# Performance work log

Hardware: AMD Instinct MI355X
Metric: run time of the kernel (lower is better)

## Reference

```python
import jax, jax.numpy as jnp
import numpy as np

H = 32          # num attention heads
KVH = 8         # num key/value heads
D = 128         # head dim
THETA = 10000.0


def _rope_tables(kv_len):
    inv_freq = 1.0 / (THETA ** (jnp.arange(0, D, 2, dtype=jnp.float32) / D))  # [D/2]
    t = jnp.arange(kv_len, dtype=jnp.float32)
    freqs = jnp.outer(t, inv_freq)                  # [kv_len, D/2]
    emb = jnp.concatenate([freqs, freqs], axis=-1)  # [kv_len, D]
    return jnp.cos(emb), jnp.sin(emb)


def _rotate_half(x):
    x1, x2 = jnp.split(x, 2, axis=-1)
    return jnp.concatenate([-x2, x1], axis=-1)


def setup_inputs() -> dict:
    key = jax.random.key(0)
    ks = jax.random.split(key, 7)
    B, QL, KVL, HID = 4, 128, 4096, 4096
    hidden_states = jax.random.normal(ks[0], (B, QL, HID), jnp.float32)
    key_states = jax.random.normal(ks[1], (B, KVH, KVL, D), jnp.float32)
    value_states = jax.random.normal(ks[2], (B, KVH, KVL, D), jnp.float32)
    Wq = jax.random.normal(ks[3], (HID, H * D), jnp.float32) * (HID ** -0.5)
    Wo = jax.random.normal(ks[4], (H * D, HID), jnp.float32) * ((H * D) ** -0.5)
    position_ids = jnp.sort(jax.random.randint(ks[5], (B, KVL), 0, KVL), axis=-1).astype(jnp.int64)
    attention_mask = jax.random.randint(ks[6], (B, 1, QL, KVL), 0, 2) == 1
    return {"hidden_states": hidden_states, "key_states": key_states,
            "value_states": value_states, "Wq": Wq, "Wo": Wo,
            "position_ids": position_ids, "attention_mask": attention_mask}


def reference(hidden_states, key_states, value_states, Wq, Wo, position_ids, attention_mask):
    B, QL, HID = hidden_states.shape
    KVL = position_ids.shape[-1]

    # q projection -> [B, H, QL, D]
    q = (hidden_states @ Wq).reshape(B, QL, H, D).transpose(0, 2, 1, 3)

    # RoPE: apply rotation for the single max position per batch to all q positions
    cos, sin = _rope_tables(KVL)                               # [KVL, D]
    pos = jnp.take_along_axis(position_ids,
                              jnp.argmax(position_ids.astype(jnp.int32), axis=1)[:, None],
                              axis=1)                          # [B, 1]
    cos_b = cos[pos][:, None]                                  # [B, 1, 1, D]
    sin_b = sin[pos][:, None]
    q = q * cos_b + _rotate_half(q) * sin_b

    # GQA repeat kv heads -> [B, H, KVL, D]
    groups = H // KVH
    k = jnp.repeat(key_states, groups, axis=1)
    v = jnp.repeat(value_states, groups, axis=1)

    scores = jnp.einsum('bhqd,bhkd->bhqk', q, k) / jnp.sqrt(jnp.float32(D))
    scores = jnp.where(attention_mask, jnp.float32(-10000.0), scores)
    attn = jax.nn.softmax(scores.astype(jnp.float32), axis=-1).astype(q.dtype)

    out = jnp.einsum('bhqk,bhkd->bhqd', attn, v)               # [B, H, QL, D]
    out = out.transpose(0, 2, 1, 3).reshape(B, QL, H * D)
    return out @ Wo
```

## Files before the change

### kernel.cpp

```cpp
#include <hip/hip_runtime.h>
#include <math.h>

typedef __attribute__((ext_vector_type(8))) short bf16x8;
typedef __attribute__((ext_vector_type(4))) float f32x4;
typedef __attribute__((ext_vector_type(4))) short s16x4;
typedef __attribute__((ext_vector_type(4))) int i32x4;

__device__ inline unsigned short f2bf(float x){
  unsigned u = __builtin_bit_cast(unsigned, x);
  u = (u + 0x7FFFu + ((u >> 16) & 1u)) >> 16;
  return (unsigned short)u;
}
__device__ inline unsigned pk2bf(float lo, float hi){
  return (unsigned)f2bf(lo) | ((unsigned)f2bf(hi) << 16);
}

__device__ inline void gl16(const void* g, void* l){
  __builtin_amdgcn_global_load_lds(
      (const __attribute__((address_space(1))) unsigned int*)g,
      (__attribute__((address_space(3))) unsigned int*)l, 16, 0, 0);
}

#define KVLEN 4096
#define QLEN  128
#define NH    32
#define NKVH  8
#define HD    128
#define HIDD  4096
#define NSPLIT 4
#define KVCHUNK (KVLEN / NSPLIT)

__global__ void prep_kernel(const int* __restrict__ pos32,
                            const unsigned int* __restrict__ mask32,
                            float* __restrict__ costab,
                            float* __restrict__ sintab,
                            int* __restrict__ flags){
  int tid = threadIdx.x;
  if (tid < 64){
    unsigned long long bal = __ballot((mask32[tid] & 0xFFFFFF00u) != 0);
    if (tid == 0) flags[0] = (bal != 0) ? 1 : 0;
  }
  int b = tid >> 6, j = tid & 63;
  bool pos64 = (pos32[2*4095 + 1] == 0);
  long long mpos;
  if (pos64) mpos = ((const long long*)pos32)[(size_t)b*KVLEN + KVLEN - 1];
  else       mpos = (long long)pos32[(size_t)b*KVLEN + KVLEN - 1];
  double inv = pow(10000.0, -((double)j) / 64.0);
  double ang = (double)mpos * inv;
  costab[b*64 + j] = (float)cos(ang);
  sintab[b*64 + j] = (float)sin(ang);
}

__global__ __launch_bounds__(256) void maskpack_kernel(const void* __restrict__ mask,
                                                       const int* __restrict__ flags,
                                                       unsigned long long* __restrict__ bits){
  int idx = blockIdx.x * 256 + threadIdx.x;
  bool m8 = (flags[0] != 0);
  bool v = m8 ? (((const unsigned char*)mask)[idx] != 0)
              : (((const int*)mask)[idx] != 0);
  unsigned long long bal = __ballot(v);
  if ((threadIdx.x & 63) == 0) bits[idx >> 6] = bal;
}

__global__ __launch_bounds__(256) void kvprep_kernel(const float* __restrict__ Kg,
                                                     const float* __restrict__ Vg,
                                                     unsigned short* __restrict__ Kswz,
                                                     unsigned short* __restrict__ V2){
  __shared__ alignas(16) char tl[16384];
  int bid = blockIdx.x;
  int tid = threadIdx.x;
  const float* kin = Kg + (size_t)bid * 8192;
  const float* vin = Vg + (size_t)bid * 8192;
  unsigned short* kout = Kswz + (size_t)bid * 8192;
  unsigned short* vout = V2   + (size_t)bid * 8192;
#pragma unroll
  for (int i = 0; i < 4; ++i){
    int c = tid + 256*i;
    int r = c >> 4, d0 = (c & 15) * 8;
    f32x4 x0 = *(const f32x4*)(kin + r*128 + d0);
    f32x4 x1 = *(const f32x4*)(kin + r*128 + d0 + 4);
    bf16x8 s;
#pragma unroll
    for (int t = 0; t < 4; ++t){ s[t] = (short)f2bf(x0[t]); s[t+4] = (short)f2bf(x1[t]); }
    unsigned o = ((unsigned)(r*256 + d0*2)) ^ (((unsigned)r & 7u) << 4);
    *(bf16x8*)(tl + o) = s;
  }
  __syncthreads();
#pragma unroll
  for (int i = 0; i < 4; ++i)
    *(bf16x8*)((char*)kout + tid*16 + i*4096) = *(const bf16x8*)(tl + tid*16 + i*4096);
#pragma unroll
  for (int i = 0; i < 4; ++i){
    int c = tid + 256*i;
    int l16 = c & 15, lk4 = (c >> 4) & 3, ks2 = (c >> 6) & 1, nf8 = c >> 7;
    int d = nf8*16 + l16;
    int kvb = ks2*32 + lk4*8;
    bf16x8 s;
#pragma unroll
    for (int e = 0; e < 8; ++e) s[e] = (short)f2bf(vin[(size_t)(kvb + e)*128 + d]);
    *(bf16x8*)(vout + (size_t)c*8) = s;
  }
}

__global__ __launch_bounds__(256) void wprep_kernel(const float* __restrict__ Wq,
                                                    const float* __restrict__ Wo,
                                                    const float* __restrict__ hidden,
                                                    unsigned short* __restrict__ WqImg,
                                                    unsigned short* __restrict__ WoImg,
                                                    unsigned short* __restrict__ A1img){
  __shared__ alignas(16) char tl[16384];
  int bid = blockIdx.x, tid = threadIdx.x;
  if (bid < 4096){
    const float* W = (bid < 2048) ? Wq : Wo;
    unsigned short* img = (bid < 2048) ? WqImg : WoImg;
    int t = bid & 2047;
    int bn = t >> 6, kt = t & 63;
    char* outB = (char*)img + (size_t)t * 16384;
#pragma unroll
    for (int i = 0; i < 4; ++i){
      int c = tid + 256*i;
      int n = c & 127, kc = c >> 7;
      const float* src = W + (size_t)(kt*64 + kc*8) * HIDD + bn*128 + n;
      bf16x8 s;
#pragma unroll
      for (int e = 0; e < 8; ++e) s[e] = (short)f2bf(src[(size_t)e * HIDD]);
      unsigned off = ((unsigned)(n*128 + kc*16)) ^ (((unsigned)n & 7u) << 4);
      *(bf16x8*)(tl + off) = s;
    }
    __syncthreads();
#pragma unroll
    for (int i = 0; i < 4; ++i)
      *(bf16x8*)(outB + tid*16 + i*4096) = *(const bf16x8*)(tl + tid*16 + i*4096);
  } else {
    int t = bid - 4096;
    int bm = t >> 6, kt = t & 63;
    char* outA = (char*)A1img + (size_t)t * 8192;
#pragma unroll
    for (int i = 0; i < 2; ++i){
      int c = tid + 256*i;
      int m = c >> 3, kc = c & 7;
      const float* src = hidden + (size_t)(bm*64 + m) * HIDD + kt*64 + kc*8;
      f32x4 x0 = *(const f32x4*)src;
      f32x4 x1 = *(const f32x4*)(src + 4);
      bf16x8 s;
#pragma unroll
      for (int e = 0; e < 4; ++e){ s[e] = (short)f2bf(x0[e]); s[e+4] = (short)f2bf(x1[e]); }
      unsigned off = ((unsigned)(m*128 + kc*16)) ^ (((unsigned)m & 7u) << 4);
      *(bf16x8*)(tl + off) = s;
    }
    __syncthreads();
#pragma unroll
    for (int i = 0; i < 2; ++i)
      *(bf16x8*)(outA + tid*16 + i*4096) = *(const bf16x8*)(tl + tid*16 + i*4096);
  }
}

template<int EPI>
__global__ __launch_bounds__(256) void gemm_kernel(const unsigned short* __restrict__ Aimg,
                                                   const unsigned short* __restrict__ Bimg,
                                                   void* __restrict__ C_,
                                                   const float* __restrict__ costab,
                                                   const float* __restrict__ sintab){
  __shared__ alignas(16) char smem[98304];
  int bid = blockIdx.x;
  int bn = (bid & 7) | ((bid >> 6) << 3);
  int bm = (bid >> 3) & 7;
  int tid = threadIdx.x, lane = tid & 63, w = tid >> 6;
  int wm = w >> 1, wn = w & 1;
  int l16 = lane & 15, lk4 = lane >> 4;
  const char* At = (const char*)Aimg + (size_t)bm * 64 * 8192;
  const char* Bt = (const char*)Bimg + (size_t)bn * 64 * 16384;
  f32x4 acc[2][4] = {};

#define GSTAGE(KT, BUF) do { \
    const char* ga_ = At + (size_t)(KT)*8192  + w*2048 + lane*16; \
    const char* gb_ = Bt + (size_t)(KT)*16384 + w*4096 + lane*16; \
    char* la_ = smem + (BUF)*24576 + w*2048; \
    char* lb_ = smem + (BUF)*24576 + 8192 + w*4096; \
    gl16(ga_, la_); gl16(ga_ + 1024, la_ + 1024); \
    _Pragma("unroll") for (int i_ = 0; i_ < 4; ++i_) gl16(gb_ + i_*1024, lb_ + i_*1024); \
  } while(0)

  GSTAGE(0, 0); GSTAGE(1, 1); GSTAGE(2, 2);

  for (int kt = 0; kt < 64; ++kt){
    if (kt + 2 < 64)      asm volatile("s_waitcnt vmcnt(12)" ::: "memory");
    else if (kt + 1 < 64) asm volatile("s_waitcnt vmcnt(6)" ::: "memory");
    else                  asm volatile("s_waitcnt vmcnt(0)" ::: "memory");
    __syncthreads();
    if (kt + 3 < 64) GSTAGE(kt + 3, (kt + 3) & 3);
    const char* Ab = smem + (kt & 3)*24576;
    const char* Bb = Ab + 8192;
    bf16x8 af[2][2];
#pragma unroll
    for (int i = 0; i < 2; ++i)
#pragma unroll
      for (int ks = 0; ks < 2; ++ks){
        unsigned m = (unsigned)(wm*32 + i*16 + l16);
        unsigned off = (m*128u + (unsigned)(ks*64 + lk4*16)) ^ ((m & 7u) << 4);
        af[i][ks] = *(const bf16x8*)(Ab + off);
      }
#pragma unroll
    for (int j = 0; j < 4; ++j)
#pragma unroll
      for (int ks = 0; ks < 2; ++ks){
        unsigned n = (unsigned)(wn*64 + j*16 + l16);
        unsigned off = (n*128u + (unsigned)(ks*64 + lk4*16)) ^ ((n & 7u) << 4);
        bf16x8 bfr = *(const bf16x8*)(Bb + off);
#pragma unroll
        for (int i = 0; i < 2; ++i)
          acc[i][j] = __builtin_amdgcn_mfma_f32_16x16x32_bf16(af[i][ks], bfr, acc[i][j], 0, 0, 0);
      }
  }
#undef GSTAGE

  if (EPI == 0){
    float* C = (float*)C_;
#pragma unroll
    for (int i = 0; i < 2; ++i)
#pragma unroll
      for (int j = 0; j < 4; ++j)
#pragma unroll
        for (int r = 0; r < 4; ++r){
          int row = bm*64 + wm*32 + i*16 + lk4*4 + r;
          int col = bn*128 + wn*64 + j*16 + l16;
          C[(size_t)row * HIDD + col] = acc[i][j][r];
        }
  } else {
    float* etile = (float*)smem;
    __syncthreads();
#pragma unroll
    for (int i = 0; i < 2; ++i)
#pragma unroll
      for (int j = 0; j < 4; ++j)
#pragma unroll
        for (int r = 0; r < 4; ++r){
          int m = wm*32 + i*16 + lk4*4 + r;
          int n = wn*64 + j*16 + l16;
          etile[m*132 + n] = acc[i][j][r];
        }
    __syncthreads();
    unsigned short* Q = (unsigned short*)C_;
    int b = bm >> 1;
    int m2 = tid & 63;
    int dh = tid >> 6;
    int ql = (bm & 1)*64 + m2;
    size_t ob = ((size_t)(b*NH + bn) * QLEN + ql) * HD;
    const float scale = 0.08838834764831845f;
#pragma unroll
    for (int dd = 0; dd < 16; ++dd){
      int d = dh*16 + dd;
      float x1 = etile[m2*132 + d];
      float x2 = etile[m2*132 + d + 64];
      float c = costab[b*64 + d];
      float s = sintab[b*64 + d];
      Q[ob + d]      = f2bf((x1*c - x2*s)*scale);
      Q[ob + d + 64] = f2bf((x2*c + x1*s)*scale);
    }
  }
}

__global__ __launch_bounds__(256, 2) void attn_kernel(const unsigned short* __restrict__ Q,
                                                      const unsigned short* __restrict__ Kswz,
                                                      const unsigned short* __restrict__ V2,
                                                      const unsigned long long* __restrict__ bits,
                                                      float* __restrict__ Opart,
                                                      float* __restrict__ Mpart,
                                                      float* __restrict__ Lpart){
  __shared__ alignas(16) unsigned short Kbuf[2][8192];
  __shared__ alignas(16) unsigned short Vbuf[2][8192];
  int bid = blockIdx.x;
  int g = (bid & 7) | ((bid >> 5) << 3);
  int j = (bid >> 3) & 3;
  int s   = g & 3;
  int kvh = (g >> 2) & 7;
  int b   = g >> 5;
  int h   = kvh * 4 + j;

  int tid = threadIdx.x, lane = tid & 63, w = tid >> 6;
  int l16 = lane & 15, lk4 = lane >> 4;
  int lk4x4 = lk4 * 4;

  bf16x8 qf[2][4];
#pragma unroll
  for (int qg = 0; qg < 2; ++qg){
    const unsigned short* qp = Q + (((size_t)(b*NH + h) * QLEN) + w*32 + qg*16 + l16) * HD;
#pragma unroll
    for (int ks = 0; ks < 4; ++ks)
      qf[qg][ks] = *(const bf16x8*)(qp + ks*32 + lk4*8);
  }
  f32x4 acc_o[2][8] = {};
  float mrun[2] = {-1e30f, -1e30f}, lrun[2] = {0.f, 0.f};

  size_t kvhbase = (size_t)(b*NKVH + kvh) * (KVLEN/64);
  const unsigned short* Ktiles = Kswz + kvhbase * 8192;
  const unsigned short* Vtiles = V2   + kvhbase * 8192;
  size_t qrow0 = (size_t)(b*QLEN + w*32 + l16);

  const int t0 = s * (KVCHUNK/64), t1 = t0 + KVCHUNK/64;
  int srcb0 = (l16 + ((lk4 & 1) << 5)) << 2;
  int srcb1 = srcb0 + 64;

#define STAGE(T, BUF) do { \
    const char* gk_ = (const char*)(Ktiles + (size_t)(T)*8192) + w*4096 + lane*16; \
    const char* gv_ = (const char*)(Vtiles + (size_t)(T)*8192) + w*4096 + lane*16; \
    char* lk_ = (char*)(&Kbuf[BUF][0]) + w*4096; \
    char* lv_ = (char*)(&Vbuf[BUF][0]) + w*4096; \
    _Pragma("unroll") for (int i_ = 0; i_ < 4; ++i_) gl16(gk_ + i_*1024, lk_ + i_*1024); \
    _Pragma("unroll") for (int i_ = 0; i_ < 4; ++i_) gl16(gv_ + i_*1024, lv_ + i_*1024); \
  } while(0)

  STAGE(t0, 0);
  int cur = 0;
  for (int t = t0; t < t1; ++t){
    asm volatile("s_waitcnt vmcnt(0)" ::: "memory");
    __syncthreads();
    if (t + 1 < t1) STAGE(t + 1, cur ^ 1);

    unsigned long long wrd[2];
    wrd[0] = bits[qrow0*64 + (size_t)t];
    wrd[1] = bits[(qrow0 + 16)*64 + (size_t)t];

    f32x4 sacc[2][4] = {};
#pragma unroll
    for (int nf = 0; nf < 4; ++nf){
      int krow = nf*16 + l16;
#pragma unroll
      for (int ks = 0; ks < 4; ++ks){
        unsigned byteoff = ((unsigned)krow*256u + (unsigned)(ks*32 + lk4*8)*2u) ^ (((unsigned)krow & 7u) << 4);
        bf16x8 kf = *(const bf16x8*)((const char*)&Kbuf[cur][0] + byteoff);
        sacc[0][nf] = __builtin_amdgcn_mfma_f32_16x16x32_bf16(kf, qf[0][ks], sacc[0][nf], 0, 0, 0);
        sacc[1][nf] = __builtin_amdgcn_mfma_f32_16x16x32_bf16(kf, qf[1][ks], sacc[1][nf], 0, 0, 0);
      }
    }

    unsigned P32[2][8];
#pragma unroll
    for (int qg = 0; qg < 2; ++qg){
      float p[4][4];
      float pm = -1e30f;
#pragma unroll
      for (int nf = 0; nf < 4; ++nf)
#pragma unroll
        for (int r = 0; r < 4; ++r){
          bool mk = (wrd[qg] >> (nf*16 + lk4x4 + r)) & 1ull;
          float sv = mk ? -10000.f : sacc[qg][nf][r];
          p[nf][r] = sv;
          pm = fmaxf(pm, sv);
        }
      pm = fmaxf(pm, __shfl_xor(pm, 16, 64));
      pm = fmaxf(pm, __shfl_xor(pm, 32, 64));
      float mnew = fmaxf(mrun[qg], pm);
      float corr = __expf(mrun[qg] - mnew);
      mrun[qg] = mnew;
      float ps = 0.f;
#pragma unroll
      for (int nf = 0; nf < 4; ++nf)
#pragma unroll
        for (int r = 0; r < 4; ++r){
          float e = __expf(p[nf][r] - mnew);
          p[nf][r] = e;
          ps += e;
        }
      ps += __shfl_xor(ps, 16, 64);
      ps += __shfl_xor(ps, 32, 64);
      lrun[qg] = lrun[qg]*corr + ps;
#pragma unroll
      for (int nf8 = 0; nf8 < 8; ++nf8)
#pragma unroll
        for (int r = 0; r < 4; ++r) acc_o[qg][nf8][r] *= corr;
#pragma unroll
      for (int nf = 0; nf < 4; ++nf){
        P32[qg][nf*2]     = pk2bf(p[nf][0], p[nf][1]);
        P32[qg][nf*2 + 1] = pk2bf(p[nf][2], p[nf][3]);
      }
    }

    bf16x8 pf[2][2];
    bool hi = lk4 >= 2;
#pragma unroll
    for (int qg = 0; qg < 2; ++qg)
#pragma unroll
      for (int ks2 = 0; ks2 < 2; ++ks2){
        int a0 = __builtin_amdgcn_ds_bpermute(srcb0, (int)P32[qg][ks2*4 + 0]);
        int b0 = __builtin_amdgcn_ds_bpermute(srcb0, (int)P32[qg][ks2*4 + 2]);
        int a1 = __builtin_amdgcn_ds_bpermute(srcb0, (int)P32[qg][ks2*4 + 1]);
        int b1 = __builtin_amdgcn_ds_bpermute(srcb0, (int)P32[qg][ks2*4 + 3]);
        int a2 = __builtin_amdgcn_ds_bpermute(srcb1, (int)P32[qg][ks2*4 + 0]);
        int b2 = __builtin_amdgcn_ds_bpermute(srcb1, (int)P32[qg][ks2*4 + 2]);
        int a3 = __builtin_amdgcn_ds_bpermute(srcb1, (int)P32[qg][ks2*4 + 1]);
        int b3 = __builtin_amdgcn_ds_bpermute(srcb1, (int)P32[qg][ks2*4 + 3]);
        i32x4 wv = { hi ? b0 : a0, hi ? b1 : a1, hi ? b2 : a2, hi ? b3 : a3 };
        pf[qg][ks2] = __builtin_bit_cast(bf16x8, wv);
      }

#pragma unroll
    for (int nf8 = 0; nf8 < 8; ++nf8)
#pragma unroll
      for (int ks2 = 0; ks2 < 2; ++ks2){
        unsigned byteoff = (unsigned)(nf8*2 + ks2)*1024u + (unsigned)lane*16u;
        bf16x8 vf = *(const bf16x8*)((const char*)&Vbuf[cur][0] + byteoff);
        acc_o[0][nf8] = __builtin_amdgcn_mfma_f32_16x16x32_bf16(vf, pf[0][ks2], acc_o[0][nf8], 0, 0, 0);
        acc_o[1][nf8] = __builtin_amdgcn_mfma_f32_16x16x32_bf16(vf, pf[1][ks2], acc_o[1][nf8], 0, 0, 0);
      }
    cur ^= 1;
  }
#undef STAGE

  size_t rowbase = ((size_t)(s*4 + b) * NH + h) * QLEN + w*32 + l16;
#pragma unroll
  for (int qg = 0; qg < 2; ++qg){
    size_t row = rowbase + qg*16;
#pragma unroll
    for (int nf8 = 0; nf8 < 8; ++nf8)
      *(f32x4*)&Opart[row * HD + nf8*16 + lk4x4] = acc_o[qg][nf8];
    if (lk4 == 0){
      Mpart[row] = mrun[qg];
      Lpart[row] = lrun[qg];
    }
  }
}

__global__ __launch_bounds__(256) void combine_kernel(const float* __restrict__ Opart,
                                                      const float* __restrict__ Mpart,
                                                      const float* __restrict__ Lpart,
                                                      unsigned short* __restrict__ A2img){
  int idx = blockIdx.x * 256 + threadIdx.x;
  int d4 = idx & 31;
  int row = idx >> 5;
  const int RS = 4 * NH * QLEN;
  float m[NSPLIT];
#pragma unroll
  for (int s = 0; s < NSPLIT; ++s) m[s] = Mpart[(size_t)s*RS + row];
  float M = fmaxf(fmaxf(m[0], m[1]), fmaxf(m[2], m[3]));
  float L = 0.f;
  f32x4 num = {};
#pragma unroll
  for (int s = 0; s < NSPLIT; ++s){
    float wsc = __expf(m[s] - M);
    L += wsc * Lpart[(size_t)s*RS + row];
    f32x4 o = *(const f32x4*)&Opart[((size_t)s*RS + row) * HD + d4*4];
#pragma unroll
    for (int t = 0; t < 4; ++t) num[t] += wsc * o[t];
  }
  int ql = row & 127, h = (row >> 7) & 31, b = row >> 12;
  int bm = b*2 + (ql >> 6), mm = ql & 63;
  int kt = h*2 + (d4 >> 4), kl = (d4*4) & 63;
  s16x4 res;
#pragma unroll
  for (int t = 0; t < 4; ++t) res[t] = (short)f2bf(num[t] / L);
  char* tile = (char*)A2img + (size_t)(bm*64 + kt) * 8192;
  unsigned off = ((unsigned)(mm*128 + kl*2)) ^ (((unsigned)mm & 7u) << 4);
  *(s16x4*)(tile + off) = res;
}

extern "C" void kernel_launch(void* const* d_in, const int* in_sizes, int n_in,
                              void* d_out, int out_size, void* d_ws, size_t ws_size,
                              hipStream_t stream){
  (void)in_sizes; (void)n_in; (void)out_size; (void)ws_size;
  const float* hidden = (const float*)d_in[0];
  const float* kst    = (const float*)d_in[1];
  const float* vst    = (const float*)d_in[2];
  const float* wq     = (const float*)d_in[3];
  const float* wo     = (const float*)d_in[4];
  const void*  pos    = d_in[5];
  const void*  mask   = d_in[6];
  float* out = (float*)d_out;

  char* ws = (char*)d_ws;
  unsigned short* Kswz  = (unsigned short*)ws;
  unsigned short* V2    = (unsigned short*)(ws + (32u << 20));
  unsigned short* WoImg = (unsigned short*)(ws + (64u << 20));
  unsigned short* WqImg = (unsigned short*)(ws + (96u << 20));
  float*          Opart = (float*)(ws + (96u << 20));
  unsigned short* A1img = (unsigned short*)(ws + (128u << 20));
  unsigned short* qbf   = (unsigned short*)(ws + (132u << 20));
  unsigned short* A2img = (unsigned short*)(ws + (136u << 20));
  float* Mpart = (float*)(ws + (140u << 20));
  float* Lpart = (float*)(ws + (140u << 20) + (256u << 10));
  unsigned long long* bits = (unsigned long long*)(ws + (140u << 20) + (512u << 10));
  float* costab = (float*)(ws + (140u << 20) + (768u << 10));
  float* sintab = costab + 256;
  int*   flags  = (int*)(sintab + 256);

  prep_kernel<<<1, 256, 0, stream>>>((const int*)pos, (const unsigned int*)mask,
                                     costab, sintab, flags);
  maskpack_kernel<<<8192, 256, 0, stream>>>(mask, flags, bits);
  kvprep_kernel<<<2048, 256, 0, stream>>>(kst, vst, Kswz, V2);
  wprep_kernel<<<4608, 256, 0, stream>>>(wq, wo, hidden, WqImg, WoImg, A1img);
  gemm_kernel<1><<<256, 256, 0, stream>>>(A1img, WqImg, qbf, costab, sintab);
  attn_kernel<<<512, 256, 0, stream>>>(qbf, Kswz, V2, bits, Opart, Mpart, Lpart);
  combine_kernel<<<2048, 256, 0, stream>>>(Opart, Mpart, Lpart, A2img);
  gemm_kernel<0><<<256, 256, 0, stream>>>(A2img, WoImg, out, nullptr, nullptr);
}
```

Before: 235.7 us.

## Move RoPE to keys, shrink GEMM tiles, restructure attention with bf16 partials

Moves the RoPE rotation out of the Q-projection epilogue and applies the inverse rotation to K during kv preparation, relying on the dot-product identity, so the Q GEMM writes scaled bf16 directly. The projection GEMMs switch to 64x64 output tiles with twice as many blocks and two blocks per CU. The attention kernel uses 512 threads with one 16-row query group per wave, skips the rescale when no row max grows, computes the row sum with a ones-vector MFMA, and stores partial outputs in bf16 to halve combine traffic. Risks include bf16 precision loss in the partials and the row sums, and extra loads of K's paired half during kvprep.

```diff
diff --git a/kernel.cpp b/kernel.cpp
--- a/kernel.cpp
+++ b/kernel.cpp
@@ -10,6 +10,9 @@
   unsigned u = __builtin_bit_cast(unsigned, x);
   u = (u + 0x7FFFu + ((u >> 16) & 1u)) >> 16;
   return (unsigned short)u;
+}
+__device__ inline float bf2f(unsigned short v){
+  return __builtin_bit_cast(float, (unsigned)v << 16);
 }
 __device__ inline unsigned pk2bf(float lo, float hi){
   return (unsigned)f2bf(lo) | ((unsigned)f2bf(hi) << 16);
@@ -64,11 +67,14 @@
 
 __global__ __launch_bounds__(256) void kvprep_kernel(const float* __restrict__ Kg,
                                                      const float* __restrict__ Vg,
+                                                     const float* __restrict__ costab,
+                                                     const float* __restrict__ sintab,
                                                      unsigned short* __restrict__ Kswz,
                                                      unsigned short* __restrict__ V2){
   __shared__ alignas(16) char tl[16384];
   int bid = blockIdx.x;
   int tid = threadIdx.x;
+  int b = bid >> 9;
   const float* kin = Kg + (size_t)bid * 8192;
   const float* vin = Vg + (size_t)bid * 8192;
   unsigned short* kout = Kswz + (size_t)bid * 8192;
@@ -77,11 +83,23 @@
   for (int i = 0; i < 4; ++i){
     int c = tid + 256*i;
     int r = c >> 4, d0 = (c & 15) * 8;
+    int dp = d0 ^ 64;
+    bool low = d0 < 64;
     f32x4 x0 = *(const f32x4*)(kin + r*128 + d0);
     f32x4 x1 = *(const f32x4*)(kin + r*128 + d0 + 4);
+    f32x4 y0 = *(const f32x4*)(kin + r*128 + dp);
+    f32x4 y1 = *(const f32x4*)(kin + r*128 + dp + 4);
+    int j0 = d0 & 63;
     bf16x8 s;
 #pragma unroll
-    for (int t = 0; t < 4; ++t){ s[t] = (short)f2bf(x0[t]); s[t+4] = (short)f2bf(x1[t]); }
+    for (int t = 0; t < 4; ++t){
+      float cc = costab[b*64 + j0 + t],     ss = sintab[b*64 + j0 + t];
+      float c2 = costab[b*64 + j0 + 4 + t], s2 = sintab[b*64 + j0 + 4 + t];
+      float v0 = low ? (x0[t]*cc + y0[t]*ss) : (x0[t]*cc - y0[t]*ss);
+      float v1 = low ? (x1[t]*c2 + y1[t]*s2) : (x1[t]*c2 - y1[t]*s2);
+      s[t] = (short)f2bf(v0);
+      s[t+4] = (short)f2bf(v1);
+    }
     unsigned o = ((unsigned)(r*256 + d0*2)) ^ (((unsigned)r & 7u) << 4);
     *(bf16x8*)(tl + o) = s;
   }
@@ -108,19 +126,19 @@
                                                     unsigned short* __restrict__ WqImg,
                                                     unsigned short* __restrict__ WoImg,
                                                     unsigned short* __restrict__ A1img){
-  __shared__ alignas(16) char tl[16384];
+  __shared__ alignas(16) char tl[8192];
   int bid = blockIdx.x, tid = threadIdx.x;
-  if (bid < 4096){
-    const float* W = (bid < 2048) ? Wq : Wo;
-    unsigned short* img = (bid < 2048) ? WqImg : WoImg;
-    int t = bid & 2047;
+  if (bid < 8192){
+    const float* W = (bid < 4096) ? Wq : Wo;
+    unsigned short* img = (bid < 4096) ? WqImg : WoImg;
+    int t = bid & 4095;
     int bn = t >> 6, kt = t & 63;
-    char* outB = (char*)img + (size_t)t * 16384;
-#pragma unroll
-    for (int i = 0; i < 4; ++i){
+    char* outB = (char*)img + (size_t)t * 8192;
+#pragma unroll
+    for (int i = 0; i < 2; ++i){
       int c = tid + 256*i;
-      int n = c & 127, kc = c >> 7;
-      const float* src = W + (size_t)(kt*64 + kc*8) * HIDD + bn*128 + n;
+      int n = c & 63, kc = c >> 6;
+      const float* src = W + (size_t)(kt*64 + kc*8) * HIDD + bn*64 + n;
       bf16x8 s;
 #pragma unroll
       for (int e = 0; e < 8; ++e) s[e] = (short)f2bf(src[(size_t)e * HIDD]);
@@ -129,10 +147,10 @@
     }
     __syncthreads();
 #pragma unroll
-    for (int i = 0; i < 4; ++i)
+    for (int i = 0; i < 2; ++i)
       *(bf16x8*)(outB + tid*16 + i*4096) = *(const bf16x8*)(tl + tid*16 + i*4096);
   } else {
-    int t = bid - 4096;
+    int t = bid - 8192;
     int bm = t >> 6, kt = t & 63;
     char* outA = (char*)A1img + (size_t)t * 8192;
 #pragma unroll
@@ -156,42 +174,40 @@
 }
 
 template<int EPI>
-__global__ __launch_bounds__(256) void gemm_kernel(const unsigned short* __restrict__ Aimg,
-                                                   const unsigned short* __restrict__ Bimg,
-                                                   void* __restrict__ C_,
-                                                   const float* __restrict__ costab,
-                                                   const float* __restrict__ sintab){
-  __shared__ alignas(16) char smem[98304];
+__global__ __launch_bounds__(256, 2) void gemm_kernel(const unsigned short* __restrict__ Aimg,
+                                                      const unsigned short* __restrict__ Bimg,
+                                                      void* __restrict__ C_){
+  __shared__ alignas(16) char smem[65536];
   int bid = blockIdx.x;
   int bn = (bid & 7) | ((bid >> 6) << 3);
   int bm = (bid >> 3) & 7;
   int tid = threadIdx.x, lane = tid & 63, w = tid >> 6;
   int wm = w >> 1, wn = w & 1;
   int l16 = lane & 15, lk4 = lane >> 4;
-  const char* At = (const char*)Aimg + (size_t)bm * 64 * 8192;
-  const char* Bt = (const char*)Bimg + (size_t)bn * 64 * 16384;
-  f32x4 acc[2][4] = {};
+  const char* At = (const char*)Aimg + (size_t)(bm*64) * 8192;
+  const char* Bt = (const char*)Bimg + (size_t)(bn*64) * 8192;
+  f32x4 acc[2][2] = {};
 
 #define GSTAGE(KT, BUF) do { \
-    const char* ga_ = At + (size_t)(KT)*8192  + w*2048 + lane*16; \
-    const char* gb_ = Bt + (size_t)(KT)*16384 + w*4096 + lane*16; \
-    char* la_ = smem + (BUF)*24576 + w*2048; \
-    char* lb_ = smem + (BUF)*24576 + 8192 + w*4096; \
+    const char* ga_ = At + (size_t)(KT)*8192 + w*2048 + lane*16; \
+    const char* gb_ = Bt + (size_t)(KT)*8192 + w*2048 + lane*16; \
+    char* la_ = smem + (BUF)*16384 + w*2048; \
+    char* lb_ = smem + (BUF)*16384 + 8192 + w*2048; \
     gl16(ga_, la_); gl16(ga_ + 1024, la_ + 1024); \
-    _Pragma("unroll") for (int i_ = 0; i_ < 4; ++i_) gl16(gb_ + i_*1024, lb_ + i_*1024); \
+    gl16(gb_, lb_); gl16(gb_ + 1024, lb_ + 1024); \
   } while(0)
 
   GSTAGE(0, 0); GSTAGE(1, 1); GSTAGE(2, 2);
 
   for (int kt = 0; kt < 64; ++kt){
-    if (kt + 2 < 64)      asm volatile("s_waitcnt vmcnt(12)" ::: "memory");
-    else if (kt + 1 < 64) asm volatile("s_waitcnt vmcnt(6)" ::: "memory");
+    if (kt + 2 < 64)      asm volatile("s_waitcnt vmcnt(8)" ::: "memory");
+    else if (kt + 1 < 64) asm volatile("s_waitcnt vmcnt(4)" ::: "memory");
     else                  asm volatile("s_waitcnt vmcnt(0)" ::: "memory");
     __syncthreads();
     if (kt + 3 < 64) GSTAGE(kt + 3, (kt + 3) & 3);
-    const char* Ab = smem + (kt & 3)*24576;
+    const char* Ab = smem + (kt & 3)*16384;
     const char* Bb = Ab + 8192;
-    bf16x8 af[2][2];
+    bf16x8 af[2][2], bfr[2][2];
 #pragma unroll
     for (int i = 0; i < 2; ++i)
 #pragma unroll
@@ -201,16 +217,20 @@
         af[i][ks] = *(const bf16x8*)(Ab + off);
       }
 #pragma unroll
-    for (int j = 0; j < 4; ++j)
+    for (int j = 0; j < 2; ++j)
 #pragma unroll
       for (int ks = 0; ks < 2; ++ks){
-        unsigned n = (unsigned)(wn*64 + j*16 + l16);
+        unsigned n = (unsigned)(wn*32 + j*16 + l16);
         unsigned off = (n*128u + (unsigned)(ks*64 + lk4*16)) ^ ((n & 7u) << 4);
-        bf16x8 bfr = *(const bf16x8*)(Bb + off);
-#pragma unroll
-        for (int i = 0; i < 2; ++i)
-          acc[i][j] = __builtin_amdgcn_mfma_f32_16x16x32_bf16(af[i][ks], bfr, acc[i][j], 0, 0, 0);
+        bfr[j][ks] = *(const bf16x8*)(Bb + off);
       }
+#pragma unroll
+    for (int i = 0; i < 2; ++i)
+#pragma unroll
+      for (int j = 0; j < 2; ++j)
+#pragma unroll
+        for (int ks = 0; ks < 2; ++ks)
+          acc[i][j] = __builtin_amdgcn_mfma_f32_16x16x32_bf16(af[i][ks], bfr[j][ks], acc[i][j], 0, 0, 0);
   }
 #undef GSTAGE
 
@@ -219,52 +239,36 @@
 #pragma unroll
     for (int i = 0; i < 2; ++i)
 #pragma unroll
-      for (int j = 0; j < 4; ++j)
+      for (int j = 0; j < 2; ++j)
 #pragma unroll
         for (int r = 0; r < 4; ++r){
           int row = bm*64 + wm*32 + i*16 + lk4*4 + r;
-          int col = bn*128 + wn*64 + j*16 + l16;
+          int col = bn*64 + wn*32 + j*16 + l16;
           C[(size_t)row * HIDD + col] = acc[i][j][r];
         }
   } else {
-    float* etile = (float*)smem;
-    __syncthreads();
-#pragma unroll
-    for (int i = 0; i < 2; ++i)
-#pragma unroll
-      for (int j = 0; j < 4; ++j)
+    unsigned short* Q = (unsigned short*)C_;
+    const float scale = 0.08838834764831845f;
+#pragma unroll
+    for (int i = 0; i < 2; ++i)
+#pragma unroll
+      for (int j = 0; j < 2; ++j)
 #pragma unroll
         for (int r = 0; r < 4; ++r){
-          int m = wm*32 + i*16 + lk4*4 + r;
-          int n = wn*64 + j*16 + l16;
-          etile[m*132 + n] = acc[i][j][r];
+          int row = bm*64 + wm*32 + i*16 + lk4*4 + r;
+          int col = bn*64 + wn*32 + j*16 + l16;
+          int b = row >> 7, ql = row & 127;
+          int h = col >> 7, d = col & 127;
+          Q[(((size_t)(b*NH + h)) * QLEN + ql) * HD + d] = f2bf(acc[i][j][r] * scale);
         }
-    __syncthreads();
-    unsigned short* Q = (unsigned short*)C_;
-    int b = bm >> 1;
-    int m2 = tid & 63;
-    int dh = tid >> 6;
-    int ql = (bm & 1)*64 + m2;
-    size_t ob = ((size_t)(b*NH + bn) * QLEN + ql) * HD;
-    const float scale = 0.08838834764831845f;
-#pragma unroll
-    for (int dd = 0; dd < 16; ++dd){
-      int d = dh*16 + dd;
-      float x1 = etile[m2*132 + d];
-      float x2 = etile[m2*132 + d + 64];
-      float c = costab[b*64 + d];
-      float s = sintab[b*64 + d];
-      Q[ob + d]      = f2bf((x1*c - x2*s)*scale);
-      Q[ob + d + 64] = f2bf((x2*c + x1*s)*scale);
-    }
-  }
-}
-
-__global__ __launch_bounds__(256, 2) void attn_kernel(const unsigned short* __restrict__ Q,
+  }
+}
+
+__global__ __launch_bounds__(512, 4) void attn_kernel(const unsigned short* __restrict__ Q,
                                                       const unsigned short* __restrict__ Kswz,
                                                       const unsigned short* __restrict__ V2,
                                                       const unsigned long long* __restrict__ bits,
-                                                      float* __restrict__ Opart,
+                                                      unsigned short* __restrict__ Opart,
                                                       float* __restrict__ Mpart,
                                                       float* __restrict__ Lpart){
   __shared__ alignas(16) unsigned short Kbuf[2][8192];
@@ -281,33 +285,37 @@
   int l16 = lane & 15, lk4 = lane >> 4;
   int lk4x4 = lk4 * 4;
 
-  bf16x8 qf[2][4];
-#pragma unroll
-  for (int qg = 0; qg < 2; ++qg){
-    const unsigned short* qp = Q + (((size_t)(b*NH + h) * QLEN) + w*32 + qg*16 + l16) * HD;
+  bf16x8 qf[4];
+  {
+    const unsigned short* qp = Q + (((size_t)(b*NH + h) * QLEN) + w*16 + l16) * HD;
 #pragma unroll
     for (int ks = 0; ks < 4; ++ks)
-      qf[qg][ks] = *(const bf16x8*)(qp + ks*32 + lk4*8);
-  }
-  f32x4 acc_o[2][8] = {};
-  float mrun[2] = {-1e30f, -1e30f}, lrun[2] = {0.f, 0.f};
+      qf[ks] = *(const bf16x8*)(qp + ks*32 + lk4*8);
+  }
+  bf16x8 vone;
+#pragma unroll
+  for (int t = 0; t < 8; ++t) vone[t] = (short)0x3F80;
+
+  f32x4 acc_o[8] = {};
+  f32x4 acc_l = {};
+  float mrun = -1e30f;
 
   size_t kvhbase = (size_t)(b*NKVH + kvh) * (KVLEN/64);
   const unsigned short* Ktiles = Kswz + kvhbase * 8192;
   const unsigned short* Vtiles = V2   + kvhbase * 8192;
-  size_t qrow0 = (size_t)(b*QLEN + w*32 + l16);
+  size_t qrow = (size_t)(b*QLEN + w*16 + l16);
 
   const int t0 = s * (KVCHUNK/64), t1 = t0 + KVCHUNK/64;
   int srcb0 = (l16 + ((lk4 & 1) << 5)) << 2;
   int srcb1 = srcb0 + 64;
 
 #define STAGE(T, BUF) do { \
-    const char* gk_ = (const char*)(Ktiles + (size_t)(T)*8192) + w*4096 + lane*16; \
-    const char* gv_ = (const char*)(Vtiles + (size_t)(T)*8192) + w*4096 + lane*16; \
-    char* lk_ = (char*)(&Kbuf[BUF][0]) + w*4096; \
-    char* lv_ = (char*)(&Vbuf[BUF][0]) + w*4096; \
-    _Pragma("unroll") for (int i_ = 0; i_ < 4; ++i_) gl16(gk_ + i_*1024, lk_ + i_*1024); \
-    _Pragma("unroll") for (int i_ = 0; i_ < 4; ++i_) gl16(gv_ + i_*1024, lv_ + i_*1024); \
+    const char* gk_ = (const char*)(Ktiles + (size_t)(T)*8192) + w*2048 + lane*16; \
+    const char* gv_ = (const char*)(Vtiles + (size_t)(T)*8192) + w*2048 + lane*16; \
+    char* lk_ = (char*)(&Kbuf[BUF][0]) + w*2048; \
+    char* lv_ = (char*)(&Vbuf[BUF][0]) + w*2048; \
+    gl16(gk_, lk_); gl16(gk_ + 1024, lk_ + 1024); \
+    gl16(gv_, lv_); gl16(gv_ + 1024, lv_ + 1024); \
   } while(0)
 
   STAGE(t0, 0);
@@ -316,12 +324,10 @@
     asm volatile("s_waitcnt vmcnt(0)" ::: "memory");
     __syncthreads();
     if (t + 1 < t1) STAGE(t + 1, cur ^ 1);
-
-    unsigned long long wrd[2];
-    wrd[0] = bits[qrow0*64 + (size_t)t];
-    wrd[1] = bits[(qrow0 + 16)*64 + (size_t)t];
-
-    f32x4 sacc[2][4] = {};
+    unsigned long long wrd = bits[qrow*64 + (size_t)t];
+    __builtin_amdgcn_sched_barrier(0);
+
+    f32x4 sacc[4] = {};
 #pragma unroll
     for (int nf = 0; nf < 4; ++nf){
       int krow = nf*16 + l16;
@@ -329,70 +335,60 @@
       for (int ks = 0; ks < 4; ++ks){
         unsigned byteoff = ((unsigned)krow*256u + (unsigned)(ks*32 + lk4*8)*2u) ^ (((unsigned)krow & 7u) << 4);
         bf16x8 kf = *(const bf16x8*)((const char*)&Kbuf[cur][0] + byteoff);
-        sacc[0][nf] = __builtin_amdgcn_mfma_f32_16x16x32_bf16(kf, qf[0][ks], sacc[0][nf], 0, 0, 0);
-        sacc[1][nf] = __builtin_amdgcn_mfma_f32_16x16x32_bf16(kf, qf[1][ks], sacc[1][nf], 0, 0, 0);
+        sacc[nf] = __builtin_amdgcn_mfma_f32_16x16x32_bf16(kf, qf[ks], sacc[nf], 0, 0, 0);
       }
     }
 
-    unsigned P32[2][8];
-#pragma unroll
-    for (int qg = 0; qg < 2; ++qg){
-      float p[4][4];
-      float pm = -1e30f;
-#pragma unroll
-      for (int nf = 0; nf < 4; ++nf)
-#pragma unroll
-        for (int r = 0; r < 4; ++r){
-          bool mk = (wrd[qg] >> (nf*16 + lk4x4 + r)) & 1ull;
-          float sv = mk ? -10000.f : sacc[qg][nf][r];
-          p[nf][r] = sv;
-          pm = fmaxf(pm, sv);
-        }
-      pm = fmaxf(pm, __shfl_xor(pm, 16, 64));
-      pm = fmaxf(pm, __shfl_xor(pm, 32, 64));
-      float mnew = fmaxf(mrun[qg], pm);
-      float corr = __expf(mrun[qg] - mnew);
-      mrun[qg] = mnew;
-      float ps = 0.f;
-#pragma unroll
-      for (int nf = 0; nf < 4; ++nf)
-#pragma unroll
-        for (int r = 0; r < 4; ++r){
-          float e = __expf(p[nf][r] - mnew);
-          p[nf][r] = e;
-          ps += e;
-        }
-      ps += __shfl_xor(ps, 16, 64);
-      ps += __shfl_xor(ps, 32, 64);
-      lrun[qg] = lrun[qg]*corr + ps;
+    float p[4][4];
+    float pm = -1e30f;
+#pragma unroll
+    for (int nf = 0; nf < 4; ++nf)
+#pragma unroll
+      for (int r = 0; r < 4; ++r){
+        bool mk = (wrd >> (nf*16 + lk4x4 + r)) & 1ull;
+        float sv = mk ? -10000.f : sacc[nf][r];
+        p[nf][r] = sv;
+        pm = fmaxf(pm, sv);
+      }
+    pm = fmaxf(pm, __shfl_xor(pm, 16, 64));
+    pm = fmaxf(pm, __shfl_xor(pm, 32, 64));
+    if (__any(pm > mrun)){
+      float mnew = fmaxf(mrun, pm);
+      float corr = __expf(mrun - mnew);
+      mrun = mnew;
 #pragma unroll
       for (int nf8 = 0; nf8 < 8; ++nf8)
 #pragma unroll
-        for (int r = 0; r < 4; ++r) acc_o[qg][nf8][r] *= corr;
-#pragma unroll
-      for (int nf = 0; nf < 4; ++nf){
-        P32[qg][nf*2]     = pk2bf(p[nf][0], p[nf][1]);
-        P32[qg][nf*2 + 1] = pk2bf(p[nf][2], p[nf][3]);
-      }
-    }
-
-    bf16x8 pf[2][2];
+        for (int r = 0; r < 4; ++r) acc_o[nf8][r] *= corr;
+#pragma unroll
+      for (int r = 0; r < 4; ++r) acc_l[r] *= corr;
+    }
+    unsigned P32[8];
+#pragma unroll
+    for (int nf = 0; nf < 4; ++nf){
+      float e0 = __expf(p[nf][0] - mrun);
+      float e1 = __expf(p[nf][1] - mrun);
+      float e2 = __expf(p[nf][2] - mrun);
+      float e3 = __expf(p[nf][3] - mrun);
+      P32[nf*2]     = pk2bf(e0, e1);
+      P32[nf*2 + 1] = pk2bf(e2, e3);
+    }
+
+    bf16x8 pf[2];
     bool hi = lk4 >= 2;
 #pragma unroll
-    for (int qg = 0; qg < 2; ++qg)
-#pragma unroll
-      for (int ks2 = 0; ks2 < 2; ++ks2){
-        int a0 = __builtin_amdgcn_ds_bpermute(srcb0, (int)P32[qg][ks2*4 + 0]);
-        int b0 = __builtin_amdgcn_ds_bpermute(srcb0, (int)P32[qg][ks2*4 + 2]);
-        int a1 = __builtin_amdgcn_ds_bpermute(srcb0, (int)P32[qg][ks2*4 + 1]);
-        int b1 = __builtin_amdgcn_ds_bpermute(srcb0, (int)P32[qg][ks2*4 + 3]);
-        int a2 = __builtin_amdgcn_ds_bpermute(srcb1, (int)P32[qg][ks2*4 + 0]);
-        int b2 = __builtin_amdgcn_ds_bpermute(srcb1, (int)P32[qg][ks2*4 + 2]);
-        int a3 = __builtin_amdgcn_ds_bpermute(srcb1, (int)P32[qg][ks2*4 + 1]);
-        int b3 = __builtin_amdgcn_ds_bpermute(srcb1, (int)P32[qg][ks2*4 + 3]);
-        i32x4 wv = { hi ? b0 : a0, hi ? b1 : a1, hi ? b2 : a2, hi ? b3 : a3 };
-        pf[qg][ks2] = __builtin_bit_cast(bf16x8, wv);
-      }
+    for (int ks2 = 0; ks2 < 2; ++ks2){
+      int a0 = __builtin_amdgcn_ds_bpermute(srcb0, (int)P32[ks2*4 + 0]);
+      int b0 = __builtin_amdgcn_ds_bpermute(srcb0, (int)P32[ks2*4 + 2]);
+      int a1 = __builtin_amdgcn_ds_bpermute(srcb0, (int)P32[ks2*4 + 1]);
+      int b1 = __builtin_amdgcn_ds_bpermute(srcb0, (int)P32[ks2*4 + 3]);
+      int a2 = __builtin_amdgcn_ds_bpermute(srcb1, (int)P32[ks2*4 + 0]);
+      int b2 = __builtin_amdgcn_ds_bpermute(srcb1, (int)P32[ks2*4 + 2]);
+      int a3 = __builtin_amdgcn_ds_bpermute(srcb1, (int)P32[ks2*4 + 1]);
+      int b3 = __builtin_amdgcn_ds_bpermute(srcb1, (int)P32[ks2*4 + 3]);
+      i32x4 wv = { hi ? b0 : a0, hi ? b1 : a1, hi ? b2 : a2, hi ? b3 : a3 };
+      pf[ks2] = __builtin_bit_cast(bf16x8, wv);
+    }
 
 #pragma unroll
     for (int nf8 = 0; nf8 < 8; ++nf8)
@@ -400,28 +396,30 @@
       for (int ks2 = 0; ks2 < 2; ++ks2){
         unsigned byteoff = (unsigned)(nf8*2 + ks2)*1024u + (unsigned)lane*16u;
         bf16x8 vf = *(const bf16x8*)((const char*)&Vbuf[cur][0] + byteoff);
-        acc_o[0][nf8] = __builtin_amdgcn_mfma_f32_16x16x32_bf16(vf, pf[0][ks2], acc_o[0][nf8], 0, 0, 0);
-        acc_o[1][nf8] = __builtin_amdgcn_mfma_f32_16x16x32_bf16(vf, pf[1][ks2], acc_o[1][nf8], 0, 0, 0);
+        acc_o[nf8] = __builtin_amdgcn_mfma_f32_16x16x32_bf16(vf, pf[ks2], acc_o[nf8], 0, 0, 0);
       }
+#pragma unroll
+    for (int ks2 = 0; ks2 < 2; ++ks2)
+      acc_l = __builtin_amdgcn_mfma_f32_16x16x32_bf16(vone, pf[ks2], acc_l, 0, 0, 0);
     cur ^= 1;
   }
 #undef STAGE
 
-  size_t rowbase = ((size_t)(s*4 + b) * NH + h) * QLEN + w*32 + l16;
-#pragma unroll
-  for (int qg = 0; qg < 2; ++qg){
-    size_t row = rowbase + qg*16;
-#pragma unroll
-    for (int nf8 = 0; nf8 < 8; ++nf8)
-      *(f32x4*)&Opart[row * HD + nf8*16 + lk4x4] = acc_o[qg][nf8];
-    if (lk4 == 0){
-      Mpart[row] = mrun[qg];
-      Lpart[row] = lrun[qg];
-    }
-  }
-}
-
-__global__ __launch_bounds__(256) void combine_kernel(const float* __restrict__ Opart,
+  size_t row = ((size_t)(s*4 + b) * NH + h) * QLEN + w*16 + l16;
+#pragma unroll
+  for (int nf8 = 0; nf8 < 8; ++nf8){
+    s16x4 o;
+#pragma unroll
+    for (int r = 0; r < 4; ++r) o[r] = (short)f2bf(acc_o[nf8][r]);
+    *(s16x4*)&Opart[row * HD + nf8*16 + lk4x4] = o;
+  }
+  if (lk4 == 0){
+    Mpart[row] = mrun;
+    Lpart[row] = acc_l[0];
+  }
+}
+
+__global__ __launch_bounds__(256) void combine_kernel(const unsigned short* __restrict__ Opart,
                                                       const float* __restrict__ Mpart,
                                                       const float* __restrict__ Lpart,
                                                       unsigned short* __restrict__ A2img){
@@ -439,9 +437,9 @@
   for (int s = 0; s < NSPLIT; ++s){
     float wsc = __expf(m[s] - M);
     L += wsc * Lpart[(size_t)s*RS + row];
-    f32x4 o = *(const f32x4*)&Opart[((size_t)s*RS + row) * HD + d4*4];
-#pragma unroll
-    for (int t = 0; t < 4; ++t) num[t] += wsc * o[t];
+    s16x4 o = *(const s16x4*)&Opart[((size_t)s*RS + row) * HD + d4*4];
+#pragma unroll
+    for (int t = 0; t < 4; ++t) num[t] += wsc * bf2f((unsigned short)o[t]);
   }
   int ql = row & 127, h = (row >> 7) & 31, b = row >> 12;
   int bm = b*2 + (ql >> 6), mm = ql & 63;
@@ -472,7 +470,7 @@
   unsigned short* V2    = (unsigned short*)(ws + (32u << 20));
   unsigned short* WoImg = (unsigned short*)(ws + (64u << 20));
   unsigned short* WqImg = (unsigned short*)(ws + (96u << 20));
-  float*          Opart = (float*)(ws + (96u << 20));
+  unsigned short* Opart = (unsigned short*)(ws + (96u << 20));
   unsigned short* A1img = (unsigned short*)(ws + (128u << 20));
   unsigned short* qbf   = (unsigned short*)(ws + (132u << 20));
   unsigned short* A2img = (unsigned short*)(ws + (136u << 20));
@@ -486,10 +484,10 @@
   prep_kernel<<<1, 256, 0, stream>>>((const int*)pos, (const unsigned int*)mask,
                                      costab, sintab, flags);
   maskpack_kernel<<<8192, 256, 0, stream>>>(mask, flags, bits);
-  kvprep_kernel<<<2048, 256, 0, stream>>>(kst, vst, Kswz, V2);
-  wprep_kernel<<<4608, 256, 0, stream>>>(wq, wo, hidden, WqImg, WoImg, A1img);
-  gemm_kernel<1><<<256, 256, 0, stream>>>(A1img, WqImg, qbf, costab, sintab);
-  attn_kernel<<<512, 256, 0, stream>>>(qbf, Kswz, V2, bits, Opart, Mpart, Lpart);
+  kvprep_kernel<<<2048, 256, 0, stream>>>(kst, vst, costab, sintab, Kswz, V2);
+  wprep_kernel<<<8704, 256, 0, stream>>>(wq, wo, hidden, WqImg, WoImg, A1img);
+  gemm_kernel<1><<<512, 256, 0, stream>>>(A1img, WqImg, qbf);
+  attn_kernel<<<512, 512, 0, stream>>>(qbf, Kswz, V2, bits, Opart, Mpart, Lpart);
   combine_kernel<<<2048, 256, 0, stream>>>(Opart, Mpart, Lpart, A2img);
-  gemm_kernel<0><<<256, 256, 0, stream>>>(A2img, WoImg, out, nullptr, nullptr);
-}
+  gemm_kernel<0><<<512, 256, 0, stream>>>(A2img, WoImg, out);
+}
```

Measured after the change: 237.7 us. About the same (+0.9%).
